# Kernel optimization log

Hardware: AMD Instinct MI355X
Metric: run time of the kernel (lower is better)

## Reference

```python
import jax, jax.numpy as jnp
import numpy as np

H = 256
EPS = 1e-5

def setup_inputs() -> dict:
    key = jax.random.key(0)
    ks = jax.random.split(key, 9)
    B, T = 2048, 512
    x = jax.random.randint(ks[0], (B, T, 1), 0, 10).astype(jnp.float32)
    # parameters (torch nn.Linear stores weight as [out,in]; we store [in,out])
    W_embed = jax.random.normal(ks[1], (1, H), jnp.float32) * 0.5
    b_embed = jax.random.normal(ks[2], (H,), jnp.float32) * 0.05
    W_update = jax.random.normal(ks[3], (H, H), jnp.float32) * (1.0 / np.sqrt(H))
    b_update = jax.random.normal(ks[4], (H,), jnp.float32) * 0.05
    gamma = jnp.ones((H,), jnp.float32)
    beta = jnp.zeros((H,), jnp.float32)
    W_out = jax.random.normal(ks[5], (H, 10), jnp.float32) * (1.0 / np.sqrt(H))
    b_out = jax.random.normal(ks[6], (10,), jnp.float32) * 0.05
    return {"x": x, "W_embed": W_embed, "b_embed": b_embed,
            "W_update": W_update, "b_update": b_update,
            "gamma": gamma, "beta": beta, "W_out": W_out, "b_out": b_out}

def _layernorm(h, gamma, beta):
    mu = jnp.mean(h, axis=-1, keepdims=True)
    var = jnp.mean(jnp.square(h - mu), axis=-1, keepdims=True)
    return (h - mu) * jax.lax.rsqrt(var + EPS) * gamma + beta

def reference(x, W_embed, b_embed, W_update, b_update, gamma, beta, W_out, b_out):
    B, T, _ = x.shape
    xt = jnp.transpose(x, (1, 0, 2))  # [T, B, 1]

    def step(h, x_t):
        inp = jnp.tanh(x_t @ W_embed + b_embed)           # [B, H]
        h = jnp.tanh((inp + h) @ W_update + b_update)     # [B, H]
        h = _layernorm(h, gamma, beta)
        return h, None

    h0 = jnp.zeros((B, H), x.dtype)
    h_final, _ = jax.lax.scan(step, h0, xt)
    return h_final @ W_out + b_out                        # [B, 10]
```

## Files before the change

### kernel.cpp

```cpp
#include <hip/hip_runtime.h>
#include <hip/hip_fp16.h>
#include <cstdint>

#define T_STEPS 512
#define HDIM    256
#define ROWS    8
#define LN_EPS  1e-5f

typedef _Float16 half8   __attribute__((ext_vector_type(8)));
typedef _Float16 half4v  __attribute__((ext_vector_type(4)));
typedef __fp16   fp16x2  __attribute__((ext_vector_type(2)));
typedef float    float4v __attribute__((ext_vector_type(4)));
typedef float    float2v __attribute__((ext_vector_type(2)));
typedef int      int4v   __attribute__((ext_vector_type(4)));
typedef int      int2v   __attribute__((ext_vector_type(2)));

#if __has_builtin(__builtin_amdgcn_permlane32_swap)
#define HAS_PL32 1
#else
#define HAS_PL32 0
#endif
#if __has_builtin(__builtin_amdgcn_permlane16_swap)
#define HAS_PL16 1
#else
#define HAS_PL16 0
#endif

struct __align__(16) Smem {
  _Float16 Bp[2][4096];
  float    gb[10][268];
  float    wg[260];
  float    wb[260];
  float    red[2][8][20];
  int      xi[8][516];
};

__device__ __forceinline__ float tanh_fast(float x) {
  float e = __expf(2.0f * x);
  float r = __builtin_amdgcn_rcpf(e + 1.0f);
  return fmaf(-2.0f, r, 1.0f);
}
__device__ __forceinline__ float dpp_ror8(float v) {
  return __int_as_float(__builtin_amdgcn_mov_dpp(__float_as_int(v), 0x128, 0xf, 0xf, true));
}
__device__ __forceinline__ float swz_xor16(float v) {
  return __int_as_float(__builtin_amdgcn_ds_swizzle(__float_as_int(v), 0x401F));
}
__device__ __forceinline__ float sum_xor16(float v) {
#if HAS_PL16
  int2v r2 = __builtin_amdgcn_permlane16_swap(__float_as_int(v), __float_as_int(v), false, false);
  return __int_as_float(r2[0]) + __int_as_float(r2[1]);
#else
  return v + swz_xor16(v);
#endif
}
__device__ __forceinline__ float sum_xor32(float v) {
#if HAS_PL32
  int2v r2 = __builtin_amdgcn_permlane32_swap(__float_as_int(v), __float_as_int(v), false, false);
  return __int_as_float(r2[0]) + __int_as_float(r2[1]);
#else
  return v + __shfl_xor(v, 32, 64);
#endif
}

__global__ __launch_bounds__(512, 1)
void rnn_scan_kernel(const float* __restrict__ x,
                     const float* __restrict__ we,  const float* __restrict__ be,
                     const float* __restrict__ Wu,  const float* __restrict__ bu,
                     const float* __restrict__ gma, const float* __restrict__ bta,
                     const float* __restrict__ Wo,  const float* __restrict__ bo,
                     float* __restrict__ out)
{
  __shared__ Smem sm;
  const int tid = threadIdx.x;
  const int wv  = tid >> 6;
  const int l   = tid & 63;
  const int q   = l >> 4;
  const int m   = l & 15;
  const int sel = m >> 3;
  const int r   = m & 7;
  const int r0  = blockIdx.x * ROWS;

  for (int i = tid; i < ROWS * T_STEPS; i += 512) {
    const int rr = i >> 9, c = i & (T_STEPS - 1);
    int xv = (int)x[(size_t)(r0 + rr) * T_STEPS + c];
    xv = xv < 0 ? 0 : (xv > 9 ? 9 : xv);
    sm.xi[rr][c] = xv;
  }
  if (tid < ROWS) {
    sm.xi[tid][512] = 0; sm.xi[tid][513] = 0;
    sm.xi[tid][514] = 0; sm.xi[tid][515] = 0;
  }

  float* et = reinterpret_cast<float*>(&sm.Bp[0][0]);
  if (tid < HDIM) {
    const float wek = we[tid], bek = be[tid];
    #pragma unroll
    for (int v = 0; v < 10; ++v)
      et[v*HDIM + tid] = tanh_fast(fmaf((float)v, wek, bek));
  }
  __syncthreads();

  {
    const int g = tid >> 8;
    const int n = tid & 255;
    float acc[5] = {0,0,0,0,0};
    float accx = 0.0f;
    const int vb = g * 5;
    for (int k = 0; k < HDIM; ++k) {
      const float wk = Wu[(size_t)k*HDIM + n];
      #pragma unroll
      for (int v = 0; v < 5; ++v) acc[v] = fmaf(et[(vb+v)*HDIM + k], wk, acc[v]);
      const float xk = g ? bta[k] : gma[k];
      accx = fmaf(xk, wk, accx);
    }
    const float bun = bu[n];
    #pragma unroll
    for (int v = 0; v < 5; ++v) sm.gb[vb+v][n] = acc[v] + bun;
    if (g == 0) sm.wg[n] = accx; else sm.wb[n] = accx;
  }
  __syncthreads();

  if (tid < HDIM) {
    const float wbn = sm.wb[tid];
    #pragma unroll
    for (int v = 0; v < 10; ++v) sm.gb[v][tid] += wbn;
  }
  {
    uint32_t* p = reinterpret_cast<uint32_t*>(&sm.Bp[0][0]);
    for (int i = tid; i < 4096; i += 512) p[i] = 0u;
  }
  if (tid < 320) (&sm.red[0][0][0])[tid] = 0.0f;

  half8 Whi[2][8], Wlo[2][8];
  #pragma unroll
  for (int nt = 0; nt < 2; ++nt) {
    const int n = wv*32 + nt*16 + m;
    #pragma unroll
    for (int kt = 0; kt < 8; ++kt) {
      const int k0 = kt*32 + q*8;
      half8 hi, lo;
      #pragma unroll
      for (int j = 0; j < 8; ++j) {
        float v = Wu[(size_t)(k0 + j)*HDIM + n];
        _Float16 h = (_Float16)v;
        hi[j] = h;
        lo[j] = (_Float16)((v - (float)h) * 2048.0f);
      }
      Whi[nt][kt] = hi; Wlo[nt][kt] = lo;
    }
  }
  const int n_sel = wv*32 + sel*16 + q*4;
  const float4v gmr = *reinterpret_cast<const float4v*>(&gma[n_sel]);
  __syncthreads();
  const float4v wgr = *reinterpret_cast<const float4v*>(&sm.wg[n_sel]);

  const float c1 = 4.8828125e-4f;
  const float* gbp = &sm.gb[0][n_sel];
  float4v th4;

  const int rdoff = l * 8;
  const int woff  = wv*512 + (2*sel + (q>>1))*128 + r*8 + (q&1)*4;

  int4v xQ = *reinterpret_cast<const int4v*>(&sm.xi[r][0]);
  float4v gbv_n = *reinterpret_cast<const float4v*>(gbp + xQ[0]*268);

  for (int k = 0; k < T_STEPS/4; ++k) {
    const int4v xQn = *reinterpret_cast<const int4v*>(&sm.xi[r][k*4 + 4]);
    #pragma unroll
    for (int e = 0; e < 4; ++e) {
      const int rb = e & 1, wb = rb ^ 1;

      const float4v pq = *reinterpret_cast<const float4v*>(&sm.red[rb][r][q*4]);

      const float4v gbv = gbv_n;
      const int xv2 = (e < 3) ? xQ[e + 1] : xQn[0];

      const _Float16* pbB = &sm.Bp[rb][rdoff];
      half8 bfr[8];
      #pragma unroll
      for (int kt = 0; kt < 8; ++kt)
        bfr[kt] = *reinterpret_cast<const half8*>(pbB + kt*512);

      float4v d10, d11, d20, d21;
      d10 = 0.0f; d11 = 0.0f; d20 = 0.0f; d21 = 0.0f;
      __builtin_amdgcn_s_setprio(1);
      #pragma unroll
      for (int kt = 0; kt < 8; ++kt) {
        d10 = __builtin_amdgcn_mfma_f32_16x16x32_f16(Whi[0][kt], bfr[kt], d10, 0, 0, 0);
        d20 = __builtin_amdgcn_mfma_f32_16x16x32_f16(Wlo[0][kt], bfr[kt], d20, 0, 0, 0);
      }
      __builtin_amdgcn_s_setprio(0);

      gbv_n = *reinterpret_cast<const float4v*>(gbp + xv2*268);
      float S  = pq[0] + pq[2];
      float Sq = pq[1] + pq[3];
      S  = sum_xor32(sum_xor16(S));
      Sq = sum_xor32(sum_xor16(Sq));
      const float mu  = S * (1.0f/256.0f);
      const float var = fmaf(Sq, 1.0f/256.0f, -mu*mu);
      const float rs  = __builtin_amdgcn_rsqf(var + LN_EPS);
      const float nrsmu = -rs * mu;
      const float rsc   = rs * c1;
      const float csA   = sel ? rsc : rs;

      __builtin_amdgcn_s_setprio(1);
      #pragma unroll
      for (int kt = 0; kt < 8; ++kt) {
        d11 = __builtin_amdgcn_mfma_f32_16x16x32_f16(Whi[1][kt], bfr[kt], d11, 0, 0, 0);
        d21 = __builtin_amdgcn_mfma_f32_16x16x32_f16(Wlo[1][kt], bfr[kt], d21, 0, 0, 0);
      }
      __builtin_amdgcn_s_setprio(0);

      float4v sendv, locv;
      #pragma unroll
      for (int i2 = 0; i2 < 4; ++i2) {
        const float pA = sel ? d10[i2] : d11[i2];
        const float pB = sel ? 0.0f    : d21[i2];
        sendv[i2] = fmaf(csA, pA, rsc * pB);
        const float qA = sel ? d11[i2] : d10[i2];
        const float qB = sel ? 0.0f    : d20[i2];
        locv[i2]  = fmaf(csA, qA, rsc * qB);
      }
      float4v recv;
      #pragma unroll
      for (int i2 = 0; i2 < 4; ++i2) recv[i2] = dpp_ror8(sendv[i2]);

      float s = 0.0f, sq = 0.0f;
      float g2v[4];
      #pragma unroll
      for (int i2 = 0; i2 < 4; ++i2) {
        const float base = fmaf(nrsmu, wgr[i2], gbv[i2]);
        const float pre  = locv[i2] + recv[i2] + base;
        const float th   = tanh_fast(pre);
        th4[i2] = th; s += th; sq = fmaf(th, th, sq);
        g2v[i2] = th * gmr[i2];
      }
      const fp16x2 h01 = __builtin_amdgcn_cvt_pkrtz(g2v[0], g2v[1]);
      const fp16x2 h23 = __builtin_amdgcn_cvt_pkrtz(g2v[2], g2v[3]);
      const float r0f = (g2v[0] - (float)h01[0]) * 2048.0f;
      const float r1f = (g2v[1] - (float)h01[1]) * 2048.0f;
      const float r2f = (g2v[2] - (float)h23[0]) * 2048.0f;
      const float r3f = (g2v[3] - (float)h23[1]) * 2048.0f;
      const fp16x2 l01 = __builtin_amdgcn_cvt_pkrtz(r0f, r1f);
      const fp16x2 l23 = __builtin_amdgcn_cvt_pkrtz(r2f, r3f);
      half4v hi4, lo4;
      hi4[0] = (_Float16)h01[0]; hi4[1] = (_Float16)h01[1];
      hi4[2] = (_Float16)h23[0]; hi4[3] = (_Float16)h23[1];
      lo4[0] = (_Float16)l01[0]; lo4[1] = (_Float16)l01[1];
      lo4[2] = (_Float16)l23[0]; lo4[3] = (_Float16)l23[1];

      s  += dpp_ror8(s);  s  = sum_xor32(sum_xor16(s));
      sq += dpp_ror8(sq); sq = sum_xor32(sum_xor16(sq));

      _Float16* wp = &sm.Bp[wb][woff];
      *reinterpret_cast<half4v*>(wp)      = hi4;
      *reinterpret_cast<half4v*>(wp + 64) = lo4;
      if (l < 8) {
        float2v v2; v2[0] = s; v2[1] = sq;
        *reinterpret_cast<float2v*>(&sm.red[wb][l][wv*2]) = v2;
      }
      __syncthreads();
    }
    xQ = xQn;
  }

  float mu, rs;
  {
    const float4v pq = *reinterpret_cast<const float4v*>(&sm.red[0][r][q*4]);
    float S  = pq[0] + pq[2];
    float Sq = pq[1] + pq[3];
    S  = sum_xor32(sum_xor16(S));
    Sq = sum_xor32(sum_xor16(Sq));
    mu = S * (1.0f/256.0f);
    const float var = fmaf(Sq, 1.0f/256.0f, -mu*mu);
    rs = __builtin_amdgcn_rsqf(var + LN_EPS);
  }
  float* hf = reinterpret_cast<float*>(&sm.gb[0][0]);
  {
    const float4v btv = *reinterpret_cast<const float4v*>(&bta[n_sel]);
    float4v h4;
    #pragma unroll
    for (int e = 0; e < 4; ++e)
      h4[e] = fmaf((th4[e] - mu) * rs, gmr[e], btv[e]);
    *reinterpret_cast<float4v*>(&hf[r*260 + n_sel]) = h4;
  }
  __syncthreads();
  if (tid < ROWS*10) {
    const int rr = tid / 10, o = tid % 10;
    float acc = bo[o];
    #pragma unroll 4
    for (int n = 0; n < HDIM; ++n)
      acc = fmaf(hf[rr*260 + n], Wo[n*10 + o], acc);
    out[(size_t)(r0 + rr)*10 + o] = acc;
  }
}

extern "C" void kernel_launch(void* const* d_in, const int* in_sizes, int n_in,
                              void* d_out, int out_size, void* d_ws, size_t ws_size,
                              hipStream_t stream) {
  const float* x  = (const float*)d_in[0];
  const float* we = (const float*)d_in[1];
  const float* be = (const float*)d_in[2];
  const float* Wu = (const float*)d_in[3];
  const float* bu = (const float*)d_in[4];
  const float* ga = (const float*)d_in[5];
  const float* bt = (const float*)d_in[6];
  const float* Wo = (const float*)d_in[7];
  const float* bo = (const float*)d_in[8];
  const int B = in_sizes[0] / T_STEPS;
  dim3 grid(B / ROWS), block(512);
  rnn_scan_kernel<<<grid, block, 0, stream>>>(x, we, be, Wu, bu, ga, bt, Wo, bo,
                                              (float*)d_out);
}
```

Baseline: 573.0 us.

## Split per-step epilogue so first n-tile finishes while second MFMA chain runs

Changes the ownership of output columns so each lane handles two columns from each of the two 16-wide n-tiles, instead of four columns from one tile. The first tile's epilogue (combine, dpp exchange, tanh, fp16 split, LDS store) now depends only on d10/d20, so it can overlap with the second tile's MFMA chain. Before, every lane had to wait for both accumulator sets. The cost is narrower half2 LDS stores and float2 parameter loads, plus a changed write layout that must still match the B-fragment read pattern.

```diff
diff --git a/kernel.cpp b/kernel.cpp
--- a/kernel.cpp
+++ b/kernel.cpp
@@ -9,6 +9,7 @@
 
 typedef _Float16 half8   __attribute__((ext_vector_type(8)));
 typedef _Float16 half4v  __attribute__((ext_vector_type(4)));
+typedef _Float16 half2v  __attribute__((ext_vector_type(2)));
 typedef __fp16   fp16x2  __attribute__((ext_vector_type(2)));
 typedef float    float4v __attribute__((ext_vector_type(4)));
 typedef float    float2v __attribute__((ext_vector_type(2)));
@@ -150,20 +151,23 @@
       Whi[nt][kt] = hi; Wlo[nt][kt] = lo;
     }
   }
-  const int n_sel = wv*32 + sel*16 + q*4;
-  const float4v gmr = *reinterpret_cast<const float4v*>(&gma[n_sel]);
+  const int nb = wv*32 + q*4 + sel*2;
+  const float2v gmr0 = *reinterpret_cast<const float2v*>(&gma[nb]);
+  const float2v gmr1 = *reinterpret_cast<const float2v*>(&gma[nb + 16]);
   __syncthreads();
-  const float4v wgr = *reinterpret_cast<const float4v*>(&sm.wg[n_sel]);
+  const float2v wgr0 = *reinterpret_cast<const float2v*>(&sm.wg[nb]);
+  const float2v wgr1 = *reinterpret_cast<const float2v*>(&sm.wg[nb + 16]);
 
   const float c1 = 4.8828125e-4f;
-  const float* gbp = &sm.gb[0][n_sel];
+  const float* gbp = &sm.gb[0][nb];
   float4v th4;
 
   const int rdoff = l * 8;
-  const int woff  = wv*512 + (2*sel + (q>>1))*128 + r*8 + (q&1)*4;
+  const int woff0 = wv*512 + (q>>1)*128 + r*8 + (q&1)*4 + sel*2;
 
   int4v xQ = *reinterpret_cast<const int4v*>(&sm.xi[r][0]);
-  float4v gbv_n = *reinterpret_cast<const float4v*>(gbp + xQ[0]*268);
+  float2v gbv0_n = *reinterpret_cast<const float2v*>(gbp + xQ[0]*268);
+  float2v gbv1_n = *reinterpret_cast<const float2v*>(gbp + xQ[0]*268 + 16);
 
   for (int k = 0; k < T_STEPS/4; ++k) {
     const int4v xQn = *reinterpret_cast<const int4v*>(&sm.xi[r][k*4 + 4]);
@@ -173,7 +177,7 @@
 
       const float4v pq = *reinterpret_cast<const float4v*>(&sm.red[rb][r][q*4]);
 
-      const float4v gbv = gbv_n;
+      const float2v gbv0 = gbv0_n, gbv1 = gbv1_n;
       const int xv2 = (e < 3) ? xQ[e + 1] : xQn[0];
 
       const _Float16* pbB = &sm.Bp[rb][rdoff];
@@ -182,8 +186,8 @@
       for (int kt = 0; kt < 8; ++kt)
         bfr[kt] = *reinterpret_cast<const half8*>(pbB + kt*512);
 
-      float4v d10, d11, d20, d21;
-      d10 = 0.0f; d11 = 0.0f; d20 = 0.0f; d21 = 0.0f;
+      float4v d10, d20;
+      d10 = 0.0f; d20 = 0.0f;
       __builtin_amdgcn_s_setprio(1);
       #pragma unroll
       for (int kt = 0; kt < 8; ++kt) {
@@ -192,7 +196,8 @@
       }
       __builtin_amdgcn_s_setprio(0);
 
-      gbv_n = *reinterpret_cast<const float4v*>(gbp + xv2*268);
+      gbv0_n = *reinterpret_cast<const float2v*>(gbp + xv2*268);
+      gbv1_n = *reinterpret_cast<const float2v*>(gbp + xv2*268 + 16);
       float S  = pq[0] + pq[2];
       float Sq = pq[1] + pq[3];
       S  = sum_xor32(sum_xor16(S));
@@ -202,8 +207,9 @@
       const float rs  = __builtin_amdgcn_rsqf(var + LN_EPS);
       const float nrsmu = -rs * mu;
       const float rsc   = rs * c1;
-      const float csA   = sel ? rsc : rs;
-
+
+      float4v d11, d21;
+      d11 = 0.0f; d21 = 0.0f;
       __builtin_amdgcn_s_setprio(1);
       #pragma unroll
       for (int kt = 0; kt < 8; ++kt) {
@@ -212,50 +218,60 @@
       }
       __builtin_amdgcn_s_setprio(0);
 
-      float4v sendv, locv;
-      #pragma unroll
-      for (int i2 = 0; i2 < 4; ++i2) {
-        const float pA = sel ? d10[i2] : d11[i2];
-        const float pB = sel ? 0.0f    : d21[i2];
-        sendv[i2] = fmaf(csA, pA, rsc * pB);
-        const float qA = sel ? d11[i2] : d10[i2];
-        const float qB = sel ? 0.0f    : d20[i2];
-        locv[i2]  = fmaf(csA, qA, rsc * qB);
-      }
-      float4v recv;
-      #pragma unroll
-      for (int i2 = 0; i2 < 4; ++i2) recv[i2] = dpp_ror8(sendv[i2]);
-
       float s = 0.0f, sq = 0.0f;
-      float g2v[4];
-      #pragma unroll
-      for (int i2 = 0; i2 < 4; ++i2) {
-        const float base = fmaf(nrsmu, wgr[i2], gbv[i2]);
-        const float pre  = locv[i2] + recv[i2] + base;
-        const float th   = tanh_fast(pre);
-        th4[i2] = th; s += th; sq = fmaf(th, th, sq);
-        g2v[i2] = th * gmr[i2];
-      }
-      const fp16x2 h01 = __builtin_amdgcn_cvt_pkrtz(g2v[0], g2v[1]);
-      const fp16x2 h23 = __builtin_amdgcn_cvt_pkrtz(g2v[2], g2v[3]);
-      const float r0f = (g2v[0] - (float)h01[0]) * 2048.0f;
-      const float r1f = (g2v[1] - (float)h01[1]) * 2048.0f;
-      const float r2f = (g2v[2] - (float)h23[0]) * 2048.0f;
-      const float r3f = (g2v[3] - (float)h23[1]) * 2048.0f;
-      const fp16x2 l01 = __builtin_amdgcn_cvt_pkrtz(r0f, r1f);
-      const fp16x2 l23 = __builtin_amdgcn_cvt_pkrtz(r2f, r3f);
-      half4v hi4, lo4;
-      hi4[0] = (_Float16)h01[0]; hi4[1] = (_Float16)h01[1];
-      hi4[2] = (_Float16)h23[0]; hi4[3] = (_Float16)h23[1];
-      lo4[0] = (_Float16)l01[0]; lo4[1] = (_Float16)l01[1];
-      lo4[2] = (_Float16)l23[0]; lo4[3] = (_Float16)l23[1];
+
+      {
+        float own0 = sel ? rsc * d10[2] : fmaf(rs, d10[0], rsc * d20[0]);
+        float own1 = sel ? rsc * d10[3] : fmaf(rs, d10[1], rsc * d20[1]);
+        float snd0 = sel ? rsc * d10[0] : fmaf(rs, d10[2], rsc * d20[2]);
+        float snd1 = sel ? rsc * d10[1] : fmaf(rs, d10[3], rsc * d20[3]);
+        const float rcv0 = dpp_ror8(snd0);
+        const float rcv1 = dpp_ror8(snd1);
+        const float pre0 = own0 + rcv0 + fmaf(nrsmu, wgr0[0], gbv0[0]);
+        const float pre1 = own1 + rcv1 + fmaf(nrsmu, wgr0[1], gbv0[1]);
+        const float t0 = tanh_fast(pre0);
+        const float t1 = tanh_fast(pre1);
+        th4[0] = t0; th4[1] = t1;
+        s += t0 + t1; sq = fmaf(t0, t0, fmaf(t1, t1, sq));
+        const float g0 = t0 * gmr0[0], g1 = t1 * gmr0[1];
+        const fp16x2 h01 = __builtin_amdgcn_cvt_pkrtz(g0, g1);
+        const float r0f = (g0 - (float)h01[0]) * 2048.0f;
+        const float r1f = (g1 - (float)h01[1]) * 2048.0f;
+        const fp16x2 l01 = __builtin_amdgcn_cvt_pkrtz(r0f, r1f);
+        half2v hi2, lo2;
+        hi2[0] = (_Float16)h01[0]; hi2[1] = (_Float16)h01[1];
+        lo2[0] = (_Float16)l01[0]; lo2[1] = (_Float16)l01[1];
+        *reinterpret_cast<half2v*>(&sm.Bp[wb][woff0])      = hi2;
+        *reinterpret_cast<half2v*>(&sm.Bp[wb][woff0 + 64]) = lo2;
+      }
+
+      {
+        float own0 = sel ? rsc * d11[2] : fmaf(rs, d11[0], rsc * d21[0]);
+        float own1 = sel ? rsc * d11[3] : fmaf(rs, d11[1], rsc * d21[1]);
+        float snd0 = sel ? rsc * d11[0] : fmaf(rs, d11[2], rsc * d21[2]);
+        float snd1 = sel ? rsc * d11[1] : fmaf(rs, d11[3], rsc * d21[3]);
+        const float rcv0 = dpp_ror8(snd0);
+        const float rcv1 = dpp_ror8(snd1);
+        const float pre0 = own0 + rcv0 + fmaf(nrsmu, wgr1[0], gbv1[0]);
+        const float pre1 = own1 + rcv1 + fmaf(nrsmu, wgr1[1], gbv1[1]);
+        const float t0 = tanh_fast(pre0);
+        const float t1 = tanh_fast(pre1);
+        th4[2] = t0; th4[3] = t1;
+        s += t0 + t1; sq = fmaf(t0, t0, fmaf(t1, t1, sq));
+        const float g0 = t0 * gmr1[0], g1 = t1 * gmr1[1];
+        const fp16x2 h01 = __builtin_amdgcn_cvt_pkrtz(g0, g1);
+        const float r0f = (g0 - (float)h01[0]) * 2048.0f;
+        const float r1f = (g1 - (float)h01[1]) * 2048.0f;
+        const fp16x2 l01 = __builtin_amdgcn_cvt_pkrtz(r0f, r1f);
+        half2v hi2, lo2;
+        hi2[0] = (_Float16)h01[0]; hi2[1] = (_Float16)h01[1];
+        lo2[0] = (_Float16)l01[0]; lo2[1] = (_Float16)l01[1];
+        *reinterpret_cast<half2v*>(&sm.Bp[wb][woff0 + 256])      = hi2;
+        *reinterpret_cast<half2v*>(&sm.Bp[wb][woff0 + 256 + 64]) = lo2;
+      }
 
       s  += dpp_ror8(s);  s  = sum_xor32(sum_xor16(s));
       sq += dpp_ror8(sq); sq = sum_xor32(sum_xor16(sq));
-
-      _Float16* wp = &sm.Bp[wb][woff];
-      *reinterpret_cast<half4v*>(wp)      = hi4;
-      *reinterpret_cast<half4v*>(wp + 64) = lo4;
       if (l < 8) {
         float2v v2; v2[0] = s; v2[1] = sq;
         *reinterpret_cast<float2v*>(&sm.red[wb][l][wv*2]) = v2;
@@ -278,12 +294,16 @@
   }
   float* hf = reinterpret_cast<float*>(&sm.gb[0][0]);
   {
-    const float4v btv = *reinterpret_cast<const float4v*>(&bta[n_sel]);
-    float4v h4;
-    #pragma unroll
-    for (int e = 0; e < 4; ++e)
-      h4[e] = fmaf((th4[e] - mu) * rs, gmr[e], btv[e]);
-    *reinterpret_cast<float4v*>(&hf[r*260 + n_sel]) = h4;
+    const float2v bt0 = *reinterpret_cast<const float2v*>(&bta[nb]);
+    const float2v bt1 = *reinterpret_cast<const float2v*>(&bta[nb + 16]);
+    float2v h0, h1;
+    #pragma unroll
+    for (int j = 0; j < 2; ++j) {
+      h0[j] = fmaf((th4[j]     - mu) * rs, gmr0[j], bt0[j]);
+      h1[j] = fmaf((th4[2 + j] - mu) * rs, gmr1[j], bt1[j]);
+    }
+    *reinterpret_cast<float2v*>(&hf[r*260 + nb])      = h0;
+    *reinterpret_cast<float2v*>(&hf[r*260 + nb + 16]) = h1;
   }
   __syncthreads();
   if (tid < ROWS*10) {
```

Result: slower. 590.1 us (+3.0%).

## Replace per-step block barrier with per-wave LDS flags and triple buffering

Applied to the files above, without the earlier changes.

Drops the __syncthreads at the end of each recurrence step. Each wave now publishes a per-step flag in LDS after writing its slice of the next hidden state, and consumers spin on the flag for each k-tile before loading it. Buffers go from double to triple so a fast wave cannot overwrite data a slow wave is still reading. Each wave also starts on a different k-tile, so it first uses its own freshly written data and waves run staggered. The cost is spin-loop polling on LDS and a reliance on LDS write ordering through s_waitcnt, which is fragile.

```diff
diff --git a/kernel.cpp b/kernel.cpp
--- a/kernel.cpp
+++ b/kernel.cpp
@@ -27,11 +27,12 @@
 #endif
 
 struct __align__(16) Smem {
-  _Float16 Bp[2][4096];
+  _Float16 Bp[3][4096];
   float    gb[10][268];
   float    wg[260];
   float    wb[260];
-  float    red[2][8][20];
+  float    red[3][8][20];
+  int      flg[3][8];
   int      xi[8][516];
 };
 
@@ -128,26 +129,32 @@
   }
   {
     uint32_t* p = reinterpret_cast<uint32_t*>(&sm.Bp[0][0]);
-    for (int i = tid; i < 4096; i += 512) p[i] = 0u;
-  }
-  if (tid < 320) (&sm.red[0][0][0])[tid] = 0.0f;
+    for (int i = tid; i < 2048; i += 512) p[i] = 0u;
+  }
+  if (tid < 160) (&sm.red[0][0][0])[tid] = 0.0f;
+  if (tid < 8) {
+    sm.flg[0][tid] = 0;
+    sm.flg[1][tid] = -1;
+    sm.flg[2][tid] = -1;
+  }
 
   half8 Whi[2][8], Wlo[2][8];
   #pragma unroll
   for (int nt = 0; nt < 2; ++nt) {
     const int n = wv*32 + nt*16 + m;
     #pragma unroll
-    for (int kt = 0; kt < 8; ++kt) {
+    for (int j = 0; j < 8; ++j) {
+      const int kt = (wv + j) & 7;
       const int k0 = kt*32 + q*8;
       half8 hi, lo;
       #pragma unroll
-      for (int j = 0; j < 8; ++j) {
-        float v = Wu[(size_t)(k0 + j)*HDIM + n];
+      for (int jj = 0; jj < 8; ++jj) {
+        float v = Wu[(size_t)(k0 + jj)*HDIM + n];
         _Float16 h = (_Float16)v;
-        hi[j] = h;
-        lo[j] = (_Float16)((v - (float)h) * 2048.0f);
-      }
-      Whi[nt][kt] = hi; Wlo[nt][kt] = lo;
+        hi[jj] = h;
+        lo[jj] = (_Float16)((v - (float)h) * 2048.0f);
+      }
+      Whi[nt][j] = hi; Wlo[nt][j] = lo;
     }
   }
   const int n_sel = wv*32 + sel*16 + q*4;
@@ -161,37 +168,43 @@
 
   const int rdoff = l * 8;
   const int woff  = wv*512 + (2*sel + (q>>1))*128 + r*8 + (q&1)*4;
+  _Float16* bpflat = &sm.Bp[0][0];
 
   int4v xQ = *reinterpret_cast<const int4v*>(&sm.xi[r][0]);
   float4v gbv_n = *reinterpret_cast<const float4v*>(gbp + xQ[0]*268);
 
+  int rbuf = 0;
   for (int k = 0; k < T_STEPS/4; ++k) {
     const int4v xQn = *reinterpret_cast<const int4v*>(&sm.xi[r][k*4 + 4]);
     #pragma unroll
     for (int e = 0; e < 4; ++e) {
-      const int rb = e & 1, wb = rb ^ 1;
-
-      const float4v pq = *reinterpret_cast<const float4v*>(&sm.red[rb][r][q*4]);
+      const int t = k*4 + e;
+      int wbuf = rbuf + 1; if (wbuf == 3) wbuf = 0;
 
       const float4v gbv = gbv_n;
       const int xv2 = (e < 3) ? xQ[e + 1] : xQn[0];
 
-      const _Float16* pbB = &sm.Bp[rb][rdoff];
-      half8 bfr[8];
-      #pragma unroll
-      for (int kt = 0; kt < 8; ++kt)
-        bfr[kt] = *reinterpret_cast<const half8*>(pbB + kt*512);
-
+      const _Float16* bbase = bpflat + rbuf*4096 + rdoff;
       float4v d10, d11, d20, d21;
       d10 = 0.0f; d11 = 0.0f; d20 = 0.0f; d21 = 0.0f;
+      #pragma unroll
+      for (int j = 0; j < 8; ++j) {
+        const int kt = (wv + j) & 7;
+        volatile int* vf = &sm.flg[rbuf][kt];
+        int fv = *vf;
+        while (fv != t) fv = *vf;
+        asm volatile("" : "+v"(fv));
+        const int dep = fv ^ t;
+        const half8 b = *reinterpret_cast<const half8*>(bbase + kt*512 + dep);
+        d10 = __builtin_amdgcn_mfma_f32_16x16x32_f16(Whi[0][j], b, d10, 0, 0, 0);
+        d20 = __builtin_amdgcn_mfma_f32_16x16x32_f16(Wlo[0][j], b, d20, 0, 0, 0);
+        d11 = __builtin_amdgcn_mfma_f32_16x16x32_f16(Whi[1][j], b, d11, 0, 0, 0);
+        d21 = __builtin_amdgcn_mfma_f32_16x16x32_f16(Wlo[1][j], b, d21, 0, 0, 0);
+      }
+
       __builtin_amdgcn_s_setprio(1);
-      #pragma unroll
-      for (int kt = 0; kt < 8; ++kt) {
-        d10 = __builtin_amdgcn_mfma_f32_16x16x32_f16(Whi[0][kt], bfr[kt], d10, 0, 0, 0);
-        d20 = __builtin_amdgcn_mfma_f32_16x16x32_f16(Wlo[0][kt], bfr[kt], d20, 0, 0, 0);
-      }
-      __builtin_amdgcn_s_setprio(0);
-
+
+      const float4v pq = *reinterpret_cast<const float4v*>(&sm.red[rbuf][r][q*4]);
       gbv_n = *reinterpret_cast<const float4v*>(gbp + xv2*268);
       float S  = pq[0] + pq[2];
       float Sq = pq[1] + pq[3];
@@ -203,14 +216,6 @@
       const float nrsmu = -rs * mu;
       const float rsc   = rs * c1;
       const float csA   = sel ? rsc : rs;
-
-      __builtin_amdgcn_s_setprio(1);
-      #pragma unroll
-      for (int kt = 0; kt < 8; ++kt) {
-        d11 = __builtin_amdgcn_mfma_f32_16x16x32_f16(Whi[1][kt], bfr[kt], d11, 0, 0, 0);
-        d21 = __builtin_amdgcn_mfma_f32_16x16x32_f16(Wlo[1][kt], bfr[kt], d21, 0, 0, 0);
-      }
-      __builtin_amdgcn_s_setprio(0);
 
       float4v sendv, locv;
       #pragma unroll
@@ -253,21 +258,26 @@
       s  += dpp_ror8(s);  s  = sum_xor32(sum_xor16(s));
       sq += dpp_ror8(sq); sq = sum_xor32(sum_xor16(sq));
 
-      _Float16* wp = &sm.Bp[wb][woff];
+      _Float16* wp = bpflat + wbuf*4096 + woff;
       *reinterpret_cast<half4v*>(wp)      = hi4;
       *reinterpret_cast<half4v*>(wp + 64) = lo4;
       if (l < 8) {
         float2v v2; v2[0] = s; v2[1] = sq;
-        *reinterpret_cast<float2v*>(&sm.red[wb][l][wv*2]) = v2;
-      }
-      __syncthreads();
+        *reinterpret_cast<float2v*>(&sm.red[wbuf][l][wv*2]) = v2;
+      }
+      asm volatile("s_waitcnt lgkmcnt(0)" ::: "memory");
+      if (l == 0) *(volatile int*)&sm.flg[wbuf][wv] = t + 1;
+      __builtin_amdgcn_s_setprio(0);
+
+      rbuf = wbuf;
     }
     xQ = xQn;
   }
 
+  __syncthreads();
   float mu, rs;
   {
-    const float4v pq = *reinterpret_cast<const float4v*>(&sm.red[0][r][q*4]);
+    const float4v pq = *reinterpret_cast<const float4v*>(&sm.red[rbuf][r][q*4]);
     float S  = pq[0] + pq[2];
     float Sq = pq[1] + pq[3];
     S  = sum_xor32(sum_xor16(S));
```

New measurement: 740.4 us. +29.2%, slower.
